# Performance work log

Measured on AMD Instinct MI355X. Metric: run time of the kernel, lower is better.

## Reference

```python
import jax, jax.numpy as jnp
import numpy as np

N = 100000
E = 1600000
IN_DIM, HID, OUT = 128, 64, 32
SLOPE = 0.1


def setup_inputs() -> dict:
    key = jax.random.key(0)
    ks = jax.random.split(key, 8)
    x = jax.random.normal(ks[0], (N, IN_DIM), dtype=jnp.float32)
    edge_index = jax.random.randint(ks[1], (2, E), 0, N, dtype=jnp.int64)
    s1 = 1.0 / np.sqrt(IN_DIM)
    s2 = 1.0 / np.sqrt(HID)
    W_l1 = jax.random.uniform(ks[2], (IN_DIM, HID), jnp.float32, -s1, s1)
    W_r1 = jax.random.uniform(ks[3], (IN_DIM, HID), jnp.float32, -s1, s1)
    b1 = jax.random.uniform(ks[4], (HID,), jnp.float32, -s1, s1)
    W_l2 = jax.random.uniform(ks[5], (HID, OUT), jnp.float32, -s2, s2)
    W_r2 = jax.random.uniform(ks[6], (HID, OUT), jnp.float32, -s2, s2)
    b2 = jax.random.uniform(ks[7], (OUT,), jnp.float32, -s2, s2)
    return {"x": x, "edge_index": edge_index,
            "W_l1": W_l1, "W_r1": W_r1, "b1": b1,
            "W_l2": W_l2, "W_r2": W_r2, "b2": b2}


def _sage_conv(h, src, dst, deg_inv, W_l, W_r, b):
    # mean-aggregate neighbor features: gather from src, scatter-add to dst
    agg = jax.ops.segment_sum(h[src], dst, num_segments=N) * deg_inv  # [N, d]
    return agg @ W_l + h @ W_r + b


def reference(x, edge_index, W_l1, W_r1, b1, W_l2, W_r2, b2):
    src, dst = edge_index[0], edge_index[1]
    deg = jax.ops.segment_sum(jnp.ones((E,), x.dtype), dst, num_segments=N)
    deg_inv = (1.0 / jnp.maximum(deg, 1.0))[:, None]  # [N, 1]
    h = jax.nn.leaky_relu(_sage_conv(x, src, dst, deg_inv, W_l1, W_r1, b1), SLOPE)
    z = jax.nn.leaky_relu(_sage_conv(h, src, dst, deg_inv, W_l2, W_r2, b2), SLOPE)
    return z
```

## Files before the change

### kernel.cpp

```cpp
#include <hip/hip_runtime.h>


constexpr int IN_DIM  = 128;
constexpr int HID     = 64;
constexpr int OUT_DIM = 32;
constexpr float SLOPE = 0.1f;
constexpr int NPB_SHIFT = 8;
constexpr int NBMAX = 512;
constexpr int CHUNK = 4096;
constexpr int SUBCAP = 4096;

typedef unsigned int uint32;
typedef unsigned short ushort16;
typedef unsigned char uchar8;
using floatx2 = __attribute__((ext_vector_type(2))) float;

__device__ inline float blo(uint32 u) { return __uint_as_float(u << 16); }
__device__ inline float bhi(uint32 u) { return __uint_as_float(u & 0xffff0000u); }
__device__ inline ushort16 f2b(float f) {
    uint32 u = __float_as_uint(f);
    u += 0x7fffu + ((u >> 16) & 1u);
    return (ushort16)(u >> 16);
}
__device__ inline uint32 pack2(float lo, float hi) {
    return (uint32)f2b(lo) | ((uint32)f2b(hi) << 16);
}
__device__ inline float lrelu(float v) { return (v > 0.f) ? v : SLOPE * v; }
__device__ inline uchar8 f2fp8(float f) {
    uint32 r = (uint32)__builtin_amdgcn_cvt_pk_fp8_f32(f, f, 0, false);
    return (uchar8)(r & 0xffu);
}
__device__ inline void addp4(float* acc, uint32 w) {
    floatx2 a = __builtin_amdgcn_cvt_pk_f32_fp8((int)w, false);
    floatx2 b = __builtin_amdgcn_cvt_pk_f32_fp8((int)w, true);
    acc[0] += a[0]; acc[1] += a[1]; acc[2] += b[0]; acc[3] += b[1];
}
__device__ inline void addq8(float* acc, uint2 u) {
    addp4(acc + 0, u.x); addp4(acc + 4, u.y);
}

__global__ __launch_bounds__(256) void prep_kernel(
    const float* __restrict__ Wl1, const float* __restrict__ Wr1,
    const float* __restrict__ Wl2, const float* __restrict__ Wr2,
    ushort16* __restrict__ Wb1, ushort16* __restrict__ Wb2,
    int* __restrict__ bhist, int* __restrict__ done) {
    const int gid = blockIdx.x * 256 + threadIdx.x;
    if (gid < NBMAX) bhist[gid] = 0;
    if (gid == NBMAX) *done = 0;
    for (int i = gid; i < 128 * 128; i += gridDim.x * 256) {
        int c = i >> 7, k = i & 127;
        Wb1[i] = f2b((c < HID) ? Wl1[k * HID + c] : Wr1[k * HID + (c - HID)]);
    }
    for (int i = gid; i < 64 * 64; i += gridDim.x * 256) {
        int c = i >> 6, k = i & 63;
        Wb2[i] = f2b((c < OUT_DIM) ? Wl2[k * OUT_DIM + c]
                                   : Wr2[k * OUT_DIM + (c - OUT_DIM)]);
    }
}

__global__ __launch_bounds__(256) void hist_scan_kernel(
    const int* __restrict__ dst, int* __restrict__ bhist,
    int* __restrict__ pbase, int* __restrict__ bcur,
    int* __restrict__ done, int E, int NB) {
    __shared__ int bh[NBMAX];
    __shared__ int s2[256];
    __shared__ int flag;
    const int tid = threadIdx.x;
    for (int i = tid; i < NBMAX; i += 256) bh[i] = 0;
    __syncthreads();
    for (int e = blockIdx.x * 256 + tid; e < E; e += gridDim.x * 256)
        atomicAdd(&bh[dst[e] >> NPB_SHIFT], 1);
    __syncthreads();
    for (int b = tid; b < NBMAX; b += 256)
        if (bh[b]) atomicAdd(&bhist[b], bh[b]);
    __threadfence();
    if (tid == 0) flag = (atomicAdd(done, 1) == (int)gridDim.x - 1) ? 1 : 0;
    __syncthreads();
    if (!flag) return;
    __threadfence();
    int v0 = atomicAdd(&bhist[2 * tid], 0);
    int v1 = atomicAdd(&bhist[2 * tid + 1], 0);
    int p0 = (v0 + 15) & ~15, p1 = (v1 + 15) & ~15;
    s2[tid] = p0 + p1; __syncthreads();
    for (int off = 1; off < 256; off <<= 1) {
        int b = (tid >= off) ? s2[tid - off] : 0;
        __syncthreads();
        s2[tid] += b;
        __syncthreads();
    }
    int base = s2[tid] - (p0 + p1);
    pbase[2 * tid]     = base;      bcur[2 * tid]     = base;
    pbase[2 * tid + 1] = base + p0; bcur[2 * tid + 1] = base + p0;
}

__global__ __launch_bounds__(256) void gemm1_part_kernel(
    const float* __restrict__ x, const ushort16* __restrict__ Wb1,
    const float* __restrict__ b1,
    const int* __restrict__ src, const int* __restrict__ dst,
    int* __restrict__ bcur, uint32* __restrict__ pairs,
    uchar8* __restrict__ xl8, ushort16* __restrict__ xr,
    int N, int E, int NB, int npart) {
    using frag = __attribute__((ext_vector_type(8))) short;
    using f32x4 = __attribute__((ext_vector_type(4))) float;
    constexpr int LDA = IN_DIM + 8;
    __shared__ union {
        struct {
            int hist[NBMAX], loff[NBMAX], cur[NBMAX], gbase[NBMAX];
            int s[256];
            ushort16 perm[CHUNK];
            ushort16 buck[CHUNK];
        } p;
        ushort16 Ash[64][LDA];
        struct { uchar8 xl[64][64]; ushort16 xr[64][64]; } o;
    } sm;
    const int tid = threadIdx.x;
    if (blockIdx.x < npart) {
        const int e0  = blockIdx.x * CHUNK;
        const int cnt = min(CHUNK, E - e0);
        for (int i = tid; i < NBMAX; i += 256) sm.p.hist[i] = 0;
        __syncthreads();
        int dreg[16];
#pragma unroll
        for (int k = 0; k < 16; ++k) {
            int i = tid + k * 256;
            if (i < cnt) {
                dreg[k] = dst[e0 + i];
                atomicAdd(&sm.p.hist[dreg[k] >> NPB_SHIFT], 1);
            }
        }
        __syncthreads();
        int a0 = sm.p.hist[2 * tid], a1 = sm.p.hist[2 * tid + 1];
        sm.p.s[tid] = a0 + a1; __syncthreads();
        for (int off = 1; off < 256; off <<= 1) {
            int t = (tid >= off) ? sm.p.s[tid - off] : 0;
            __syncthreads();
            sm.p.s[tid] += t;
            __syncthreads();
        }
        int ex = sm.p.s[tid] - (a0 + a1);
        sm.p.loff[2 * tid] = ex;      sm.p.loff[2 * tid + 1] = ex + a0;
        sm.p.cur[2 * tid]  = ex;      sm.p.cur[2 * tid + 1]  = ex + a0;
        __syncthreads();
#pragma unroll
        for (int k = 0; k < 16; ++k) {
            int i = tid + k * 256;
            if (i < cnt) {
                int b = dreg[k] >> NPB_SHIFT;
                int pos = atomicAdd(&sm.p.cur[b], 1);
                sm.p.perm[pos] = (ushort16)i;
                sm.p.buck[pos] = (ushort16)b;
            }
        }
        __syncthreads();
        for (int bb = tid; bb < NB; bb += 256) {
            int b = bb + (int)blockIdx.x;
            if (b >= NB) b -= NB;
            if (b >= NB) b -= NB;
            int cb = sm.p.hist[b];
            if (cb) sm.p.gbase[b] = atomicAdd(&bcur[b], cb);
        }
        __syncthreads();
        for (int i = tid; i < cnt; i += 256) {
            int pidx = sm.p.perm[i];
            int b    = sm.p.buck[i];
            int sv = src[e0 + pidx];
            int dv = dst[e0 + pidx];
            pairs[sm.p.gbase[b] + (i - sm.p.loff[b])] =
                (uint32)sv | ((uint32)(dv & 255) << 24);
        }
        return;
    }
    const int n0 = (blockIdx.x - npart) * 64;
    {
        const int lc = (tid & 31) * 4;
        for (int row = tid >> 5; row < 64; row += 8) {
            int node = n0 + row;
            float4 xv = (node < N)
                ? *reinterpret_cast<const float4*>(&x[(long)node * IN_DIM + lc])
                : float4{0.f, 0.f, 0.f, 0.f};
            ushort16 pk[4] = {f2b(xv.x), f2b(xv.y), f2b(xv.z), f2b(xv.w)};
            *reinterpret_cast<ushort2*>(&sm.Ash[row][lc])     = ushort2{pk[0], pk[1]};
            *reinterpret_cast<ushort2*>(&sm.Ash[row][lc + 2]) = ushort2{pk[2], pk[3]};
        }
    }
    __syncthreads();
    const int lane = tid & 63;
    const int m0   = (tid >> 6) * 16;
    const int mlo  = lane & 15;
    const int qk   = lane >> 4;
    frag Af[4];
#pragma unroll
    for (int kc = 0; kc < 4; ++kc)
        Af[kc] = *reinterpret_cast<const frag*>(&sm.Ash[m0 + mlo][kc * 32 + qk * 8]);
    __syncthreads();
#pragma unroll
    for (int ct = 0; ct < 8; ++ct) {
        f32x4 acc = {0.f, 0.f, 0.f, 0.f};
#pragma unroll
        for (int kc = 0; kc < 4; ++kc) {
            frag Bf = *reinterpret_cast<const frag*>(
                &Wb1[(ct * 16 + mlo) * 128 + kc * 32 + qk * 8]);
            acc = __builtin_amdgcn_mfma_f32_16x16x32_bf16(Af[kc], Bf, acc, 0, 0, 0);
        }
        const int col = ct * 16 + mlo;
#pragma unroll
        for (int r = 0; r < 4; ++r) {
            int row = m0 + qk * 4 + r;
            if (col < HID) sm.o.xl[row][col] = f2fp8(acc[r]);
            else           sm.o.xr[row][col - HID] = f2b(acc[r] + b1[col - HID]);
        }
    }
    __syncthreads();
    for (int idx = tid; idx < 64 * 4; idx += 256) {
        int row = idx >> 2, ch = idx & 3;
        int node = n0 + row;
        if (node < N)
            reinterpret_cast<uint4*>(xl8)[(long)node * 4 + ch] =
                reinterpret_cast<const uint4*>(&sm.o.xl[0][0])[idx];
    }
    for (int idx = tid; idx < 64 * 8; idx += 256) {
        int row = idx >> 3, ch = idx & 7;
        int node = n0 + row;
        if (node < N)
            reinterpret_cast<uint4*>(xr)[(long)node * 8 + ch] =
                reinterpret_cast<const uint4*>(&sm.o.xr[0][0])[idx];
    }
}

__global__ __launch_bounds__(512) void agg1_gemm2_kernel(
    const uint32* __restrict__ pairs, const int* __restrict__ bhist,
    const int* __restrict__ pbase,
    const uint2* __restrict__ xlq, const uint4* __restrict__ xrq,
    const ushort16* __restrict__ Wb2, const float* __restrict__ b2,
    uint32* __restrict__ srcs, int* __restrict__ rowptr, int* __restrict__ degA,
    uchar8* __restrict__ hl8, ushort16* __restrict__ hr, int N) {
    using frag = __attribute__((ext_vector_type(8))) short;
    using f32x4 = __attribute__((ext_vector_type(4))) float;
    constexpr int LDH = HID + 8;
    __shared__ int hist[256], loff[256], cur[128];
    __shared__ int lsrc[SUBCAP];
    __shared__ ushort16 hsh[128][LDH];
    const int tid  = threadIdx.x;
    const int bkt  = blockIdx.x >> 1;
    const int half = blockIdx.x & 1;
    const int n0   = bkt << NPB_SHIFT;
    const int base = pbase[bkt];
    const int sz   = bhist[bkt];
    if (tid < 256) hist[tid] = 0;
    __syncthreads();
    for (int i = tid; i < sz; i += 512)
        atomicAdd(&hist[pairs[base + i] >> 24], 1);
    __syncthreads();
    int v = (tid < 256) ? hist[tid] : 0;
    if (tid < 256) loff[tid] = v;
    __syncthreads();
    for (int off = 1; off < 256; off <<= 1) {
        int t = (tid >= off && tid < 256) ? loff[tid - off] : 0;
        __syncthreads();
        if (tid < 256) loff[tid] += t;
        __syncthreads();
    }
    if (tid < 256) loff[tid] -= v;
    __syncthreads();
    if (half == 0 && tid < 256 && n0 + tid < N) {
        rowptr[n0 + tid] = base + loff[tid];
        degA[n0 + tid]   = hist[tid];
    }
    const int hbase = loff[half << 7];
    const int hcnt  = (half ? sz : loff[128]) - hbase;
    if (tid < 128) cur[tid] = loff[(half << 7) + tid] - hbase;
    __syncthreads();
    for (int i = tid; i < sz; i += 512) {
        uint32 u = pairs[base + i];
        int dl = u >> 24;
        if ((dl >> 7) == half) {
            int pos = atomicAdd(&cur[dl & 127], 1);
            lsrc[pos] = (int)(u & 0xFFFFFFu);
        }
    }
    __syncthreads();
    for (int i = tid; i < hcnt; i += 512)
        srcs[base + hbase + i] = (uint32)lsrc[i];
    const int lane = tid & 63;
    const int wid  = tid >> 6;
    const int li   = lane & 7;
#pragma unroll
    for (int pass = 0; pass < 2; ++pass) {
        const int nll = pass * 64 + wid * 8 + (lane >> 3);
        const int nl  = (half << 7) + nll;
        const int n   = n0 + nl;
        if (n >= N) continue;
        const int lo0 = loff[nl] - hbase;
        const int d   = hist[nl];
        float acc[8] = {};
        int j = 0;
        while (j + 16 <= d) {
            int i0[8], i1[8];
#pragma unroll
            for (int t = 0; t < 8; ++t) i0[t] = lsrc[lo0 + j + t];
#pragma unroll
            for (int t = 0; t < 8; ++t) i1[t] = lsrc[lo0 + j + 8 + t];
            uint2 u0[8], u1[8];
#pragma unroll
            for (int t = 0; t < 8; ++t) u0[t] = xlq[(long)i0[t] * 8 + li];
#pragma unroll
            for (int t = 0; t < 8; ++t) u1[t] = xlq[(long)i1[t] * 8 + li];
#pragma unroll
            for (int t = 0; t < 8; ++t) { addq8(acc, u0[t]); addq8(acc, u1[t]); }
            j += 16;
        }
        if (j + 8 <= d) {
            int i0[8];
#pragma unroll
            for (int t = 0; t < 8; ++t) i0[t] = lsrc[lo0 + j + t];
            uint2 u0[8];
#pragma unroll
            for (int t = 0; t < 8; ++t) u0[t] = xlq[(long)i0[t] * 8 + li];
#pragma unroll
            for (int t = 0; t < 8; ++t) addq8(acc, u0[t]);
            j += 8;
        }
        for (; j < d; ++j) {
            uint2 u = xlq[(long)lsrc[lo0 + j] * 8 + li];
            addq8(acc, u);
        }
        const float dinv = (d > 0) ? (1.f / (float)d) : 1.f;
        uint4 xv = xrq[(long)n * 8 + li];
        float h[8];
        h[0] = fmaf(acc[0], dinv, blo(xv.x)); h[1] = fmaf(acc[1], dinv, bhi(xv.x));
        h[2] = fmaf(acc[2], dinv, blo(xv.y)); h[3] = fmaf(acc[3], dinv, bhi(xv.y));
        h[4] = fmaf(acc[4], dinv, blo(xv.z)); h[5] = fmaf(acc[5], dinv, bhi(xv.z));
        h[6] = fmaf(acc[6], dinv, blo(xv.w)); h[7] = fmaf(acc[7], dinv, bhi(xv.w));
#pragma unroll
        for (int t = 0; t < 8; ++t) h[t] = lrelu(h[t]);
        uint4 pk;
        pk.x = pack2(h[0], h[1]); pk.y = pack2(h[2], h[3]);
        pk.z = pack2(h[4], h[5]); pk.w = pack2(h[6], h[7]);
        *reinterpret_cast<uint4*>(&hsh[nll][li * 8]) = pk;
    }
    __syncthreads();
    unsigned char* hl_st = reinterpret_cast<unsigned char*>(lsrc);
    ushort16* hr_st = reinterpret_cast<ushort16*>(lsrc + 1024);
    const int m0  = wid * 16;
    const int mlo = lane & 15;
    const int qk  = lane >> 4;
    frag Af[2];
#pragma unroll
    for (int kc = 0; kc < 2; ++kc)
        Af[kc] = *reinterpret_cast<const frag*>(&hsh[m0 + mlo][kc * 32 + qk * 8]);
#pragma unroll
    for (int ct = 0; ct < 4; ++ct) {
        f32x4 acc = {0.f, 0.f, 0.f, 0.f};
#pragma unroll
        for (int kc = 0; kc < 2; ++kc) {
            frag Bf = *reinterpret_cast<const frag*>(
                &Wb2[(ct * 16 + mlo) * 64 + kc * 32 + qk * 8]);
            acc = __builtin_amdgcn_mfma_f32_16x16x32_bf16(Af[kc], Bf, acc, 0, 0, 0);
        }
        const int col = ct * 16 + mlo;
#pragma unroll
        for (int r = 0; r < 4; ++r) {
            int row = m0 + qk * 4 + r;
            if (col < OUT_DIM) hl_st[row * 32 + col] = f2fp8(acc[r]);
            else hr_st[row * 32 + (col - OUT_DIM)] = f2b(acc[r] + b2[col - OUT_DIM]);
        }
    }
    __syncthreads();
    for (int idx = tid; idx < 128 * 2; idx += 512) {
        int row = idx >> 1, ch = idx & 1;
        int node = n0 + (half << 7) + row;
        if (node < N)
            reinterpret_cast<uint4*>(hl8)[(long)node * 2 + ch] =
                reinterpret_cast<const uint4*>(hl_st)[idx];
    }
    for (int idx = tid; idx < 128 * 4; idx += 512) {
        int row = idx >> 2, ch = idx & 3;
        int node = n0 + (half << 7) + row;
        if (node < N)
            reinterpret_cast<uint4*>(hr)[(long)node * 4 + ch] =
                reinterpret_cast<const uint4*>(hr_st)[idx];
    }
}

__global__ __launch_bounds__(256) void agg2_final_kernel(
    const int* __restrict__ rowptr, const int* __restrict__ degA,
    const uint32* __restrict__ srcs,
    const uint2* __restrict__ hlq, const uint4* __restrict__ hrq,
    float* __restrict__ z, int N) {
    const int lane  = threadIdx.x & 63;
    const int li    = lane & 3;
    const int gbase = lane & 60;
    const int wave  = (blockIdx.x << 2) + (threadIdx.x >> 6);
    const int n     = wave * 16 + (lane >> 2);
    if (n >= N) return;
    const int rp = rowptr[n];
    const int d  = degA[n];
    float acc[8] = {};
    int j = 0;
    while (j + 16 <= d) {
        int sA = (int)srcs[rp + j + li];
        int sB = (int)srcs[rp + j + 4 + li];
        int sC = (int)srcs[rp + j + 8 + li];
        int sD = (int)srcs[rp + j + 12 + li];
        uint2 u[16];
#pragma unroll
        for (int t = 0; t < 4; ++t) u[t]      = hlq[(long)__shfl(sA, gbase + t) * 4 + li];
#pragma unroll
        for (int t = 0; t < 4; ++t) u[4 + t]  = hlq[(long)__shfl(sB, gbase + t) * 4 + li];
#pragma unroll
        for (int t = 0; t < 4; ++t) u[8 + t]  = hlq[(long)__shfl(sC, gbase + t) * 4 + li];
#pragma unroll
        for (int t = 0; t < 4; ++t) u[12 + t] = hlq[(long)__shfl(sD, gbase + t) * 4 + li];
#pragma unroll
        for (int t = 0; t < 16; ++t) addq8(acc, u[t]);
        j += 16;
    }
    while (j + 4 <= d) {
        int sA = (int)srcs[rp + j + li];
        uint2 u[4];
#pragma unroll
        for (int t = 0; t < 4; ++t) u[t] = hlq[(long)__shfl(sA, gbase + t) * 4 + li];
#pragma unroll
        for (int t = 0; t < 4; ++t) addq8(acc, u[t]);
        j += 4;
    }
    int r = d - j;
    if (r > 0) {
        int sA = (int)srcs[rp + j + ((li < r) ? li : 0)];
#pragma unroll
        for (int t = 0; t < 3; ++t) {
            if (t < r) {
                uint2 u = hlq[(long)__shfl(sA, gbase + t) * 4 + li];
                addq8(acc, u);
            }
        }
    }
    const float dinv = (d > 0) ? (1.f / (float)d) : 1.f;
    uint4 hv = hrq[(long)n * 4 + li];
    float4 vA, vB;
    vA.x = lrelu(fmaf(acc[0], dinv, blo(hv.x))); vA.y = lrelu(fmaf(acc[1], dinv, bhi(hv.x)));
    vA.z = lrelu(fmaf(acc[2], dinv, blo(hv.y))); vA.w = lrelu(fmaf(acc[3], dinv, bhi(hv.y)));
    vB.x = lrelu(fmaf(acc[4], dinv, blo(hv.z))); vB.y = lrelu(fmaf(acc[5], dinv, bhi(hv.z)));
    vB.z = lrelu(fmaf(acc[6], dinv, blo(hv.w))); vB.w = lrelu(fmaf(acc[7], dinv, bhi(hv.w)));
    *reinterpret_cast<float4*>(&z[(long)n * OUT_DIM + 8 * li]) = vA;
    *reinterpret_cast<float4*>(&z[(long)n * OUT_DIM + 8 * li + 4]) = vB;
}

extern "C" void kernel_launch(void* const* d_in, const int* in_sizes, int n_in,
                              void* d_out, int out_size, void* d_ws, size_t ws_size,
                              hipStream_t stream) {
    const float* x   = (const float*)d_in[0];
    const int*   ei  = (const int*)d_in[1];
    const float* Wl1 = (const float*)d_in[2];
    const float* Wr1 = (const float*)d_in[3];
    const float* b1  = (const float*)d_in[4];
    const float* Wl2 = (const float*)d_in[5];
    const float* Wr2 = (const float*)d_in[6];
    const float* b2  = (const float*)d_in[7];

    const int N = in_sizes[0] / IN_DIM;
    const int E = in_sizes[1] / 2;
    const int* src = ei;
    const int* dst = ei + E;
    const int NB = (N + 255) >> NPB_SHIFT;

    char* p = (char*)d_ws;
    int* bhist    = (int*)p;           p += sizeof(int) * NBMAX;
    int* done     = (int*)p;           p += sizeof(int) * 4;
    int* pbase    = (int*)p;           p += sizeof(int) * NBMAX;
    int* bcur     = (int*)p;           p += sizeof(int) * NBMAX;
    int* rowptr   = (int*)p;           p += sizeof(int) * (N + 4);
    int* degA     = (int*)p;           p += sizeof(int) * (N + 4);
    uint32* pairs = (uint32*)p;        p += sizeof(uint32) * ((size_t)E + 16 * NBMAX);
    uint32* srcs  = (uint32*)p;        p += sizeof(uint32) * ((size_t)E + 16 * NBMAX);
    ushort16* Wb1 = (ushort16*)p;      p += sizeof(ushort16) * 128 * 128;
    ushort16* Wb2 = (ushort16*)p;      p += sizeof(ushort16) * 64 * 64;
    uchar8* xl8   = (uchar8*)p;        p += sizeof(uchar8) * ((size_t)N * HID + 64);
    ushort16* xr  = (ushort16*)p;      p += sizeof(ushort16) * ((size_t)N * HID + 8);
    uchar8* hl8   = (uchar8*)p;        p += sizeof(uchar8) * ((size_t)N * OUT_DIM + 64);
    ushort16* hr  = (ushort16*)p;      p += sizeof(ushort16) * ((size_t)N * OUT_DIM + 8);

    const int ngemm = (N + 63) / 64;
    const int npart = (E + CHUNK - 1) / CHUNK;
    prep_kernel<<<32, 256, 0, stream>>>(Wl1, Wr1, Wl2, Wr2, Wb1, Wb2, bhist, done);
    hist_scan_kernel<<<256, 256, 0, stream>>>(dst, bhist, pbase, bcur, done, E, NB);
    gemm1_part_kernel<<<npart + ngemm, 256, 0, stream>>>(
        x, Wb1, b1, src, dst, bcur, pairs, xl8, xr, N, E, NB, npart);
    agg1_gemm2_kernel<<<NB * 2, 512, 0, stream>>>(pairs, bhist, pbase,
                                                  (const uint2*)xl8, (const uint4*)xr,
                                                  Wb2, b2,
                                                  srcs, rowptr, degA, hl8, hr, N);
    agg2_final_kernel<<<(N + 63) / 64, 256, 0, stream>>>(rowptr, degA, srcs,
                                                         (const uint2*)hl8,
                                                         (const uint4*)hr,
                                                         (float*)d_out, N);
}
```

Measured before the change: 244.4 us.

## Split fused sort/aggregate kernel into sort and per-64-node gather-GEMM kernels

The fused bucket-sort + layer-1 aggregation + GEMM2 kernel is split in two. A sort kernel only writes the CSR (srcs, rowptr, degA). A new gather_gemm2 kernel then runs with 256-thread blocks over 64 nodes each, reading back its slice of srcs into LDS. The aim is more, smaller blocks with less LDS each, for better occupancy and load balance during the memory-bound gather. The cost is an extra launch and a global round trip of the source indices. Neighbour lists longer than GCAP (2048) per 64-node tile would be silently truncated.

Measured after the change: 238.2 us. -2.5%, faster.

```diff
diff --git a/kernel.cpp b/kernel.cpp
--- a/kernel.cpp
+++ b/kernel.cpp
@@ -9,6 +9,7 @@
 constexpr int NBMAX = 512;
 constexpr int CHUNK = 4096;
 constexpr int SUBCAP = 4096;
+constexpr int GCAP  = 2048;
 
 typedef unsigned int uint32;
 typedef unsigned short ushort16;
@@ -227,19 +228,13 @@
     }
 }
 
-__global__ __launch_bounds__(512) void agg1_gemm2_kernel(
+__global__ __launch_bounds__(512) void sort_kernel(
     const uint32* __restrict__ pairs, const int* __restrict__ bhist,
     const int* __restrict__ pbase,
-    const uint2* __restrict__ xlq, const uint4* __restrict__ xrq,
-    const ushort16* __restrict__ Wb2, const float* __restrict__ b2,
     uint32* __restrict__ srcs, int* __restrict__ rowptr, int* __restrict__ degA,
-    uchar8* __restrict__ hl8, ushort16* __restrict__ hr, int N) {
-    using frag = __attribute__((ext_vector_type(8))) short;
-    using f32x4 = __attribute__((ext_vector_type(4))) float;
-    constexpr int LDH = HID + 8;
+    int N) {
     __shared__ int hist[256], loff[256], cur[128];
     __shared__ int lsrc[SUBCAP];
-    __shared__ ushort16 hsh[128][LDH];
     const int tid  = threadIdx.x;
     const int bkt  = blockIdx.x >> 1;
     const int half = blockIdx.x & 1;
@@ -281,17 +276,45 @@
     __syncthreads();
     for (int i = tid; i < hcnt; i += 512)
         srcs[base + hbase + i] = (uint32)lsrc[i];
+}
+
+__global__ __launch_bounds__(256) void gather_gemm2_kernel(
+    const uint32* __restrict__ srcs, const int* __restrict__ rowptr,
+    const int* __restrict__ degA,
+    const uint2* __restrict__ xlq, const uint4* __restrict__ xrq,
+    const ushort16* __restrict__ Wb2, const float* __restrict__ b2,
+    uchar8* __restrict__ hl8, ushort16* __restrict__ hr, int N) {
+    using frag = __attribute__((ext_vector_type(8))) short;
+    using f32x4 = __attribute__((ext_vector_type(4))) float;
+    constexpr int LDH = HID + 8;
+    __shared__ int rps[64], dgs[64];
+    __shared__ int lsrc[GCAP];
+    __shared__ ushort16 hsh[64][LDH];
+    const int tid = threadIdx.x;
+    const int n0  = blockIdx.x * 64;
+    if (tid < 64) {
+        int nn = n0 + tid;
+        rps[tid] = (nn < N) ? rowptr[nn] : 0;
+        dgs[tid] = (nn < N) ? degA[nn] : 0;
+    }
+    __syncthreads();
+    const int nvalid = min(64, N - n0);
+    const int rp0 = rps[0];
+    int sz = rps[nvalid - 1] + dgs[nvalid - 1] - rp0;
+    if (sz > GCAP) sz = GCAP;
+    for (int i = tid; i < sz; i += 256)
+        lsrc[i] = (int)srcs[rp0 + i];
+    __syncthreads();
     const int lane = tid & 63;
     const int wid  = tid >> 6;
     const int li   = lane & 7;
 #pragma unroll
     for (int pass = 0; pass < 2; ++pass) {
-        const int nll = pass * 64 + wid * 8 + (lane >> 3);
-        const int nl  = (half << 7) + nll;
-        const int n   = n0 + nl;
+        const int nl = pass * 32 + wid * 8 + (lane >> 3);
+        const int n  = n0 + nl;
         if (n >= N) continue;
-        const int lo0 = loff[nl] - hbase;
-        const int d   = hist[nl];
+        const int lo0 = rps[nl] - rp0;
+        const int d   = dgs[nl];
         float acc[8] = {};
         int j = 0;
         while (j + 16 <= d) {
@@ -336,11 +359,11 @@
         uint4 pk;
         pk.x = pack2(h[0], h[1]); pk.y = pack2(h[2], h[3]);
         pk.z = pack2(h[4], h[5]); pk.w = pack2(h[6], h[7]);
-        *reinterpret_cast<uint4*>(&hsh[nll][li * 8]) = pk;
+        *reinterpret_cast<uint4*>(&hsh[nl][li * 8]) = pk;
     }
     __syncthreads();
     unsigned char* hl_st = reinterpret_cast<unsigned char*>(lsrc);
-    ushort16* hr_st = reinterpret_cast<ushort16*>(lsrc + 1024);
+    ushort16* hr_st = reinterpret_cast<ushort16*>(lsrc + 512);
     const int m0  = wid * 16;
     const int mlo = lane & 15;
     const int qk  = lane >> 4;
@@ -366,16 +389,16 @@
         }
     }
     __syncthreads();
-    for (int idx = tid; idx < 128 * 2; idx += 512) {
+    for (int idx = tid; idx < 64 * 2; idx += 256) {
         int row = idx >> 1, ch = idx & 1;
-        int node = n0 + (half << 7) + row;
+        int node = n0 + row;
         if (node < N)
             reinterpret_cast<uint4*>(hl8)[(long)node * 2 + ch] =
                 reinterpret_cast<const uint4*>(hl_st)[idx];
     }
-    for (int idx = tid; idx < 128 * 4; idx += 512) {
+    for (int idx = tid; idx < 64 * 4; idx += 256) {
         int row = idx >> 2, ch = idx & 3;
-        int node = n0 + (half << 7) + row;
+        int node = n0 + row;
         if (node < N)
             reinterpret_cast<uint4*>(hr)[(long)node * 4 + ch] =
                 reinterpret_cast<const uint4*>(hr_st)[idx];
@@ -486,10 +509,11 @@
     hist_scan_kernel<<<256, 256, 0, stream>>>(dst, bhist, pbase, bcur, done, E, NB);
     gemm1_part_kernel<<<npart + ngemm, 256, 0, stream>>>(
         x, Wb1, b1, src, dst, bcur, pairs, xl8, xr, N, E, NB, npart);
-    agg1_gemm2_kernel<<<NB * 2, 512, 0, stream>>>(pairs, bhist, pbase,
-                                                  (const uint2*)xl8, (const uint4*)xr,
-                                                  Wb2, b2,
-                                                  srcs, rowptr, degA, hl8, hr, N);
+    sort_kernel<<<NB * 2, 512, 0, stream>>>(pairs, bhist, pbase,
+                                            srcs, rowptr, degA, N);
+    gather_gemm2_kernel<<<(N + 63) / 64, 256, 0, stream>>>(
+        srcs, rowptr, degA, (const uint2*)xl8, (const uint4*)xr,
+        Wb2, b2, hl8, hr, N);
     agg2_final_kernel<<<(N + 63) / 64, 256, 0, stream>>>(rowptr, degA, srcs,
                                                          (const uint2*)hl8,
                                                          (const uint4*)hr,
```
